# Kernel tuning notes

Hardware: AMD Instinct MI355X
Metric: run time of the kernel (lower is better)

The kernel has to match this reference:

```python
import jax, jax.numpy as jnp
import numpy as np
import math

B, S, D, H = 4, 2048, 1024, 16
HD = D // H  # 64


def setup_inputs() -> dict:
    key = jax.random.key(0)
    ks = jax.random.split(key, 12)
    s_in = 1.0 / math.sqrt(D)
    inp = {
        "x_v": jax.random.normal(ks[0], (B, S, D), jnp.float32),
        "x_k": jax.random.normal(ks[1], (B, S, D), jnp.float32),
        "x_q": jax.random.normal(ks[2], (B, S, D), jnp.float32),
        "mask": jax.random.randint(ks[3], (B, S, S), 0, 2, jnp.int32),
        "Wq": jax.random.normal(ks[4], (H, D, HD), jnp.float32) * s_in,
        "bq": jax.random.normal(ks[5], (H, HD), jnp.float32) * s_in,
        "Wk": jax.random.normal(ks[6], (H, D, HD), jnp.float32) * s_in,
        "bk": jax.random.normal(ks[7], (H, HD), jnp.float32) * s_in,
        "Wv": jax.random.normal(ks[8], (H, D, HD), jnp.float32) * s_in,
        "bv": jax.random.normal(ks[9], (H, HD), jnp.float32) * s_in,
        "Wo": jax.random.normal(ks[10], (D, D), jnp.float32) * s_in,
        "bo": jax.random.normal(ks[11], (D,), jnp.float32) * s_in,
    }
    return inp


def reference(x_v, x_k, x_q, mask, Wq, bq, Wk, bk, Wv, bv, Wo, bo):
    # Batched per-head projections: [B,S,D] x [H,D,E] -> [B,H,S,E]
    q = jnp.einsum("bsd,hde->bhse", x_q, Wq) + bq[None, :, None, :]
    k = jnp.einsum("bsd,hde->bhse", x_k, Wk) + bk[None, :, None, :]
    v = jnp.einsum("bsd,hde->bhse", x_v, Wv) + bv[None, :, None, :]
    scale = 1.0 / math.sqrt(HD)
    scores = jnp.einsum("bhqe,bhke->bhqk", q, k) * scale  # [B,H,Sq,Sk]
    # Faithful to original: masked positions are set to 0 (not -inf) BEFORE softmax
    scores = jnp.where(mask[:, None, :, :] == 0, 0.0, scores)
    attn = jax.nn.softmax(scores, axis=-1)
    z = jnp.einsum("bhqk,bhke->bhqe", attn, v)  # [B,H,Sq,E]
    # Concat over heads in head order (matches torch.cat along dim=2)
    z = z.transpose(0, 2, 1, 3).reshape(B, S, D)
    return z @ Wo + bo
```

## Files before the change

### kernel.cpp

```cpp
#include <hip/hip_runtime.h>

typedef unsigned short u16;
typedef unsigned long long u64;
typedef __attribute__((ext_vector_type(8))) short bf16x8;
typedef __attribute__((ext_vector_type(4))) float f32x4;

#define LD 72
#define C_SCALE 0.18033688011112043f

__device__ __forceinline__ u16 f2b(float x) {
  union { float f; unsigned u; } c; c.f = x;
  unsigned r = (c.u + 0x7fffu + ((c.u >> 16) & 1u)) >> 16;
  return (u16)r;
}

__device__ __forceinline__ unsigned pk2(float a, float b) {
#if __has_builtin(__builtin_amdgcn_cvt_pk_bf16_f32)
  typedef __attribute__((ext_vector_type(2))) __bf16 b2;
  b2 r = __builtin_amdgcn_cvt_pk_bf16_f32(a, b);
  union { b2 v; unsigned u; } c; c.v = r;
  return c.u;
#else
  union { float f; unsigned u; } x, y;
  x.f = a; y.f = b;
  return ((x.u + 0x8000u) >> 16) | ((y.u + 0x8000u) & 0xffff0000u);
#endif
}

__device__ __forceinline__ void gll16(const u16* g, u16* l) {
  __builtin_amdgcn_global_load_lds(
      (const __attribute__((address_space(1))) void*)g,
      (__attribute__((address_space(3))) void*)l, 16, 0, 0);
}

__global__ __launch_bounds__(256) void cvt_bf16_3(
    const float4* __restrict__ s0, const float4* __restrict__ s1,
    const float4* __restrict__ s2, ushort4* __restrict__ d0,
    ushort4* __restrict__ d1, ushort4* __restrict__ d2, int n4) {
  const int z = blockIdx.y;
  const float4* src = z == 0 ? s0 : z == 1 ? s1 : s2;
  ushort4* dst = z == 0 ? d0 : z == 1 ? d1 : d2;
  int stride = gridDim.x * 256;
  for (int i = blockIdx.x * 256 + threadIdx.x; i < n4; i += stride) {
    float4 v = src[i];
    ushort4 o = { f2b(v.x), f2b(v.y), f2b(v.z), f2b(v.w) };
    dst[i] = o;
  }
}

__global__ __launch_bounds__(256) void transpose_cvt_all(
    const float* __restrict__ Wq, const float* __restrict__ Wk,
    const float* __restrict__ Wv, const float* __restrict__ Wo,
    u16* __restrict__ wq_t, u16* __restrict__ wk_t,
    u16* __restrict__ wv_t, u16* __restrict__ wo_t) {
  __shared__ u16 tile[64][65];
  const int id = blockIdx.x;
  const int which = id >> 8, sub = id & 255;
  const float* s;
  u16* d;
  int R, C, r0, c0;
  if (which < 3) {
    const float* W = which == 0 ? Wq : which == 1 ? Wk : Wv;
    u16* D = which == 0 ? wq_t : which == 1 ? wk_t : wv_t;
    int h = sub >> 4, rt = sub & 15;
    s = W + (size_t)h * 1024 * 64;
    d = D + (size_t)h * 64 * 1024;
    R = 1024; C = 64; r0 = rt * 64; c0 = 0;
  } else {
    s = Wo; d = wo_t;
    R = 1024; C = 1024; r0 = ((sub >> 4) & 15) * 64; c0 = (sub & 15) * 64;
  }
  const int t = threadIdx.x;
#pragma unroll
  for (int rep = 0; rep < 16; ++rep) {
    int idx = rep * 256 + t;
    int i = idx >> 6, j = idx & 63;
    tile[j][i] = f2b(s[(size_t)(r0 + i) * C + c0 + j]);
  }
  __syncthreads();
#pragma unroll
  for (int rep = 0; rep < 16; ++rep) {
    int idx = rep * 256 + t;
    int jj = idx >> 6, ii = idx & 63;
    d[(size_t)(c0 + jj) * R + r0 + ii] = tile[jj][ii];
  }
}

__global__ __launch_bounds__(256) void pack_mask(
    const int* __restrict__ m, u64* __restrict__ mp) {
  const int nw = (gridDim.x * 256) >> 6;
  const int wid = (blockIdx.x * 256 + threadIdx.x) >> 6;
  const int lane = threadIdx.x & 63;
  const int total = 4 * 2048 * 32;
  for (int i = wid; i < total; i += nw) {
    int v = m[(size_t)i * 64 + lane];
    u64 bits = __ballot(v != 0);
    if (lane == 0) mp[i] = bits;
  }
}

__device__ __forceinline__ void gemm_core(
    const u16* __restrict__ A, const u16* __restrict__ W,
    u16* Asm, u16* Bsm, int s0, int n0, int wv, int lane,
    int m16, int q4, f32x4 acc[4][4]) {
  const int rsub = lane >> 3, csub = lane & 7;
  const int wr = (wv & 1) * 64, wc = (wv >> 1) * 64;
  for (int k0 = 0; k0 < 1024; k0 += 64) {
    __syncthreads();
#pragma unroll
    for (int i = 0; i < 4; ++i) {
      int chunk = wv * 4 + i;
      gll16(A + (size_t)(s0 + chunk * 8 + rsub) * 1024 + k0 + csub * 8,
            Asm + chunk * 512 + lane * 8);
      gll16(W + (size_t)(n0 + chunk * 8 + rsub) * 1024 + k0 + csub * 8,
            Bsm + chunk * 512 + lane * 8);
    }
    __syncthreads();
#pragma unroll
    for (int ks = 0; ks < 2; ++ks) {
      bf16x8 af[4], bfr[4];
#pragma unroll
      for (int i = 0; i < 4; ++i)
        af[i] = *(const bf16x8*)(Asm + (wr + i * 16 + m16) * 64 + ks * 32 + q4 * 8);
#pragma unroll
      for (int j = 0; j < 4; ++j)
        bfr[j] = *(const bf16x8*)(Bsm + (wc + j * 16 + m16) * 64 + ks * 32 + q4 * 8);
#pragma unroll
      for (int i = 0; i < 4; ++i)
#pragma unroll
        for (int j = 0; j < 4; ++j)
          acc[i][j] = __builtin_amdgcn_mfma_f32_16x16x32_bf16(af[i], bfr[j], acc[i][j], 0, 0, 0);
    }
  }
}

__global__ __launch_bounds__(256, 2) void qkv_gemm(
    const u16* __restrict__ xq, const u16* __restrict__ xk,
    const u16* __restrict__ xv, const u16* __restrict__ wq,
    const u16* __restrict__ wk, const u16* __restrict__ wv_,
    const float* __restrict__ bq, const float* __restrict__ bk,
    const float* __restrict__ bv, u16* __restrict__ qb,
    u16* __restrict__ kb, u16* __restrict__ vtb) {
  __shared__ u16 S[17408];
  u16* Asm = S;
  u16* Bsm = S + 8192;
  const int z = blockIdx.z;
  const u16* A = z == 0 ? xq : z == 1 ? xk : xv;
  const u16* W = z == 0 ? wq : z == 1 ? wk : wv_;
  const float* bias = z == 0 ? bq : z == 1 ? bk : bv;
  const int s0 = blockIdx.x * 128, n0 = blockIdx.y * 128;
  const int t = threadIdx.x, wvi = t >> 6, lane = t & 63;
  const int m16 = lane & 15, q4 = lane >> 4;
  const int wr = (wvi & 1) * 64, wc = (wvi >> 1) * 64;
  f32x4 acc[4][4];
#pragma unroll
  for (int i = 0; i < 4; ++i)
#pragma unroll
    for (int j = 0; j < 4; ++j) acc[i][j] = (f32x4){0.f, 0.f, 0.f, 0.f};

  gemm_core(A, W, Asm, Bsm, s0, n0, wvi, lane, m16, q4, acc);

  if (z < 2) {
    u16* out = z == 0 ? qb : kb;
    const float scale = z == 0 ? C_SCALE : 1.0f;
#pragma unroll
    for (int j = 0; j < 4; ++j) {
      int n = n0 + wc + j * 16 + m16;
      int h = n >> 6, e = n & 63;
      float bval = bias[n];
#pragma unroll
      for (int i = 0; i < 4; ++i)
#pragma unroll
        for (int r = 0; r < 4; ++r) {
          int s = s0 + wr + i * 16 + q4 * 4 + r;
          int bi = s >> 11, sl = s & 2047;
          out[((size_t)(bi * 16 + h) * 2048 + sl) * 64 + e] =
              f2b((acc[i][j][r] + bval) * scale);
        }
    }
  } else {
    __syncthreads();
#pragma unroll
    for (int j = 0; j < 4; ++j) {
      int nl = wc + j * 16 + m16;
      float bval = bias[n0 + nl];
#pragma unroll
      for (int i = 0; i < 4; ++i)
#pragma unroll
        for (int r = 0; r < 4; ++r)
          S[nl * 136 + wr + i * 16 + q4 * 4 + r] = f2b(acc[i][j][r] + bval);
    }
    __syncthreads();
    const int bi = s0 >> 11, sl0 = s0 & 2047;
#pragma unroll
    for (int rep = 0; rep < 8; ++rep) {
      int u = rep * 256 + t;
      int rr = u >> 4, cc = (u & 15) * 8;
      int n = n0 + rr, h = n >> 6, e = n & 63;
      *(int4*)(vtb + ((size_t)(bi * 16 + h) * 64 + e) * 2048 + sl0 + cc) =
          *(const int4*)(S + rr * 136 + cc);
    }
  }
}

__global__ __launch_bounds__(256, 2) void out_gemm(
    const u16* __restrict__ Z, const u16* __restrict__ Wot,
    const float* __restrict__ bo, float* __restrict__ out) {
  __shared__ u16 S[17408];
  u16* Asm = S;
  u16* Bsm = S + 8192;
  const int s0 = blockIdx.x * 128, n0 = blockIdx.y * 128;
  const int t = threadIdx.x, wvi = t >> 6, lane = t & 63;
  const int m16 = lane & 15, q4 = lane >> 4;
  const int wr = (wvi & 1) * 64, wc = (wvi >> 1) * 64;
  f32x4 acc[4][4];
#pragma unroll
  for (int i = 0; i < 4; ++i)
#pragma unroll
    for (int j = 0; j < 4; ++j) acc[i][j] = (f32x4){0.f, 0.f, 0.f, 0.f};

  gemm_core(Z, Wot, Asm, Bsm, s0, n0, wvi, lane, m16, q4, acc);

#pragma unroll
  for (int j = 0; j < 4; ++j) {
    int n = n0 + wc + j * 16 + m16;
    float bval = bo[n];
#pragma unroll
    for (int i = 0; i < 4; ++i)
#pragma unroll
      for (int r = 0; r < 4; ++r) {
        int s = s0 + wr + i * 16 + q4 * 4 + r;
        out[(size_t)s * 1024 + n] = acc[i][j][r] + bval;
      }
  }
}

__global__ __launch_bounds__(256, 4) void attn(
    const u16* __restrict__ qb, const u16* __restrict__ kb,
    const u16* __restrict__ vt, const u64* __restrict__ mp,
    u16* __restrict__ zb) {
  __shared__ u16 Kl[2][64 * LD];
  __shared__ u16 Vl[2][64 * LD];
  const int id = blockIdx.x;
  const int qi = id >> 6;
  const int bh = id & 63;
  const int b = bh >> 4, h = bh & 15;
  const int t = threadIdx.x, w = t >> 6, lane = t & 63;
  const int m16 = lane & 15, q4 = lane >> 4;
  const size_t bho = (size_t)bh * 2048;
  const u16* qp = qb + bho * 64;
  const u16* kp = kb + bho * 64;
  const u16* vp = vt + bho * 64;
  const int qbase = qi * 128 + w * 32;

  bf16x8 qa[2][2];
#pragma unroll
  for (int qg = 0; qg < 2; ++qg)
#pragma unroll
    for (int ks = 0; ks < 2; ++ks)
      qa[qg][ks] = *(const bf16x8*)(qp + (size_t)(qbase + qg * 16 + m16) * 64 + ks * 32 + q4 * 8);

  f32x4 oacc[2][4], lacc[2];
#pragma unroll
  for (int qg = 0; qg < 2; ++qg) {
    lacc[qg] = (f32x4){0.f, 0.f, 0.f, 0.f};
#pragma unroll
    for (int g = 0; g < 4; ++g) oacc[qg][g] = (f32x4){0.f, 0.f, 0.f, 0.f};
  }
  bf16x8 ones;
#pragma unroll
  for (int j = 0; j < 8; ++j) ones[j] = (short)0x3f80;

  const u64* mpq0 = mp + ((size_t)b * 2048 + qbase + m16) * 32;
  const u64* mpq1 = mp + ((size_t)b * 2048 + qbase + 16 + m16) * 32;

  const int ch = t & 7, rw = t >> 3;
  const int sK = (((rw >> 2) & 1) * 16) + (((rw >> 3) & 3) * 4) + (rw & 3);

  int4 pk0 = *(const int4*)(kp + (size_t)rw * 64 + ch * 8);
  int4 pk1 = *(const int4*)(kp + (size_t)(rw + 32) * 64 + ch * 8);
  int4 pv0 = *(const int4*)(vp + (size_t)rw * 2048 + ch * 8);
  int4 pv1 = *(const int4*)(vp + (size_t)(rw + 32) * 2048 + ch * 8);
  u64 mb0 = mpq0[0], mb1 = mpq1[0];
  *(int4*)(&Kl[0][sK * LD + ch * 8]) = pk0;
  *(int4*)(&Kl[0][(sK + 32) * LD + ch * 8]) = pk1;
  *(int4*)(&Vl[0][rw * LD + ch * 8]) = pv0;
  *(int4*)(&Vl[0][(rw + 32) * LD + ch * 8]) = pv1;
  __syncthreads();

  for (int kt = 0; kt < 32; ++kt) {
    const int cur = kt & 1;
    u64 nmb0, nmb1;
    if (kt < 31) {
      const int k0n = (kt + 1) * 64;
      pk0 = *(const int4*)(kp + (size_t)(k0n + rw) * 64 + ch * 8);
      pk1 = *(const int4*)(kp + (size_t)(k0n + rw + 32) * 64 + ch * 8);
      pv0 = *(const int4*)(vp + (size_t)rw * 2048 + k0n + ch * 8);
      pv1 = *(const int4*)(vp + (size_t)(rw + 32) * 2048 + k0n + ch * 8);
      nmb0 = mpq0[kt + 1];
      nmb1 = mpq1[kt + 1];
    }

#pragma unroll
    for (int bb = 0; bb < 2; ++bb) {
      bf16x8 kf00 = *(const bf16x8*)(&Kl[cur][(bb * 32 + m16) * LD + q4 * 8]);
      bf16x8 kf01 = *(const bf16x8*)(&Kl[cur][(bb * 32 + m16) * LD + 32 + q4 * 8]);
      bf16x8 kf10 = *(const bf16x8*)(&Kl[cur][(bb * 32 + 16 + m16) * LD + q4 * 8]);
      bf16x8 kf11 = *(const bf16x8*)(&Kl[cur][(bb * 32 + 16 + m16) * LD + 32 + q4 * 8]);
      const unsigned by0 = (unsigned)(mb0 >> (bb * 32 + q4 * 8)) & 0xFFu;
      const unsigned by1 = (unsigned)(mb1 >> (bb * 32 + q4 * 8)) & 0xFFu;
      bf16x8 pa[2];
#pragma unroll
      for (int qg = 0; qg < 2; ++qg) {
        f32x4 sa = (f32x4){0.f, 0.f, 0.f, 0.f};
        f32x4 sb = (f32x4){0.f, 0.f, 0.f, 0.f};
        sa = __builtin_amdgcn_mfma_f32_16x16x32_bf16(kf00, qa[qg][0], sa, 0, 0, 0);
        sa = __builtin_amdgcn_mfma_f32_16x16x32_bf16(kf01, qa[qg][1], sa, 0, 0, 0);
        sb = __builtin_amdgcn_mfma_f32_16x16x32_bf16(kf10, qa[qg][0], sb, 0, 0, 0);
        sb = __builtin_amdgcn_mfma_f32_16x16x32_bf16(kf11, qa[qg][1], sb, 0, 0, 0);
        const unsigned by = qg ? by1 : by0;
        float p[8];
#pragma unroll
        for (int r = 0; r < 4; ++r) {
          p[r] = __builtin_amdgcn_exp2f((by & (1u << r)) ? sa[r] : 0.f);
          p[4 + r] = __builtin_amdgcn_exp2f((by & (1u << (4 + r))) ? sb[r] : 0.f);
        }
        union { unsigned u[4]; bf16x8 v; } pu;
        pu.u[0] = pk2(p[0], p[1]);
        pu.u[1] = pk2(p[2], p[3]);
        pu.u[2] = pk2(p[4], p[5]);
        pu.u[3] = pk2(p[6], p[7]);
        pa[qg] = pu.v;
        lacc[qg] = __builtin_amdgcn_mfma_f32_16x16x32_bf16(pa[qg], ones, lacc[qg], 0, 0, 0);
      }
#pragma unroll
      for (int e = 0; e < 4; ++e) {
        bf16x8 vf = *(const bf16x8*)(&Vl[cur][(e * 16 + m16) * LD + bb * 32 + q4 * 8]);
        oacc[0][e] = __builtin_amdgcn_mfma_f32_16x16x32_bf16(pa[0], vf, oacc[0][e], 0, 0, 0);
        oacc[1][e] = __builtin_amdgcn_mfma_f32_16x16x32_bf16(pa[1], vf, oacc[1][e], 0, 0, 0);
      }
    }

    if (kt < 31) {
      const int nxt = cur ^ 1;
      *(int4*)(&Kl[nxt][sK * LD + ch * 8]) = pk0;
      *(int4*)(&Kl[nxt][(sK + 32) * LD + ch * 8]) = pk1;
      *(int4*)(&Vl[nxt][rw * LD + ch * 8]) = pv0;
      *(int4*)(&Vl[nxt][(rw + 32) * LD + ch * 8]) = pv1;
      mb0 = nmb0;
      mb1 = nmb1;
      __syncthreads();
    }
  }

#pragma unroll
  for (int qg = 0; qg < 2; ++qg) {
#pragma unroll
    for (int r = 0; r < 4; ++r) {
      float inv = 1.f / lacc[qg][r];
      size_t zr = ((size_t)b * 2048 + qbase + qg * 16 + q4 * 4 + r) * 1024 + h * 64;
#pragma unroll
      for (int e = 0; e < 4; ++e) {
        zb[zr + e * 16 + m16] = f2b(oacc[qg][e][r] * inv);
      }
    }
  }
}

extern "C" void kernel_launch(void* const* d_in, const int* in_sizes, int n_in,
                              void* d_out, int out_size, void* d_ws, size_t ws_size,
                              hipStream_t stream) {
  const float* x_v = (const float*)d_in[0];
  const float* x_k = (const float*)d_in[1];
  const float* x_q = (const float*)d_in[2];
  const int* mask = (const int*)d_in[3];
  const float* Wq = (const float*)d_in[4];
  const float* bq = (const float*)d_in[5];
  const float* Wk = (const float*)d_in[6];
  const float* bk = (const float*)d_in[7];
  const float* Wv = (const float*)d_in[8];
  const float* bv = (const float*)d_in[9];
  const float* Wo = (const float*)d_in[10];
  const float* bo = (const float*)d_in[11];
  float* out = (float*)d_out;

  char* ws = (char*)d_ws;
  size_t off = 0;
  auto alloc_u16 = [&](size_t n) {
    u16* p = (u16*)(ws + off);
    off += n * sizeof(u16);
    return p;
  };
  u16* wq_t = alloc_u16((size_t)16 * 64 * 1024);
  u16* wk_t = alloc_u16((size_t)16 * 64 * 1024);
  u16* wv_t = alloc_u16((size_t)16 * 64 * 1024);
  u16* wo_t = alloc_u16((size_t)1024 * 1024);
  u16* qb = alloc_u16((size_t)8192 * 1024);
  u16* kb = alloc_u16((size_t)8192 * 1024);
  u16* vtb = alloc_u16((size_t)8192 * 1024);
  u16* xq16 = alloc_u16((size_t)8192 * 1024);
  u16* xk16 = alloc_u16((size_t)8192 * 1024);
  u16* xv16 = alloc_u16((size_t)8192 * 1024);
  u64* mp = (u64*)(ws + off);
  off += (size_t)262144 * 8;
  u16* zb = xq16;

  transpose_cvt_all<<<dim3(1024), 256, 0, stream>>>(
      Wq, Wk, Wv, Wo, wq_t, wk_t, wv_t, wo_t);
  pack_mask<<<dim3(1024), 256, 0, stream>>>(mask, mp);
  const int n4 = 8192 * 1024 / 4;
  cvt_bf16_3<<<dim3(512, 3), 256, 0, stream>>>(
      (const float4*)x_q, (const float4*)x_k, (const float4*)x_v,
      (ushort4*)xq16, (ushort4*)xk16, (ushort4*)xv16, n4);
  qkv_gemm<<<dim3(64, 8, 3), 256, 0, stream>>>(
      xq16, xk16, xv16, wq_t, wk_t, wv_t, bq, bk, bv, qb, kb, vtb);
  attn<<<dim3(1024), 256, 0, stream>>>(qb, kb, vtb, mp, zb);
  out_gemm<<<dim3(64, 8), 256, 0, stream>>>(zb, wo_t, bo, out);
}
```

Before: 420.7 us.

## Expand mask to bf16 multipliers instead of packed bits in attention

Replaces the bit-packed mask with a bf16 mask expanded to 1.0 or 0.0 per element. The attention kernel now loads int4 mask vectors per tile and applies the mask by multiplying scores before exp2, instead of selecting on extracted bits. This removes the per-element shift-and-test work, but grows the mask from about 2 MB to about 32 MB, and every head re-reads it. The expanded mask reuses the freed xk16/xv16 workspace. The qkv_gemm occupancy hint is also raised from 2 to 3 blocks.

```diff
diff --git a/kernel.cpp b/kernel.cpp
--- a/kernel.cpp
+++ b/kernel.cpp
@@ -25,6 +25,13 @@
   x.f = a; y.f = b;
   return ((x.u + 0x8000u) >> 16) | ((y.u + 0x8000u) & 0xffff0000u);
 #endif
+}
+
+__device__ __forceinline__ float blo(int w) {
+  union { int i; float f; } c; c.i = w << 16; return c.f;
+}
+__device__ __forceinline__ float bhi(int w) {
+  union { int i; float f; } c; c.i = w & 0xffff0000; return c.f;
 }
 
 __device__ __forceinline__ void gll16(const u16* g, u16* l) {
@@ -86,16 +93,14 @@
   }
 }
 
-__global__ __launch_bounds__(256) void pack_mask(
-    const int* __restrict__ m, u64* __restrict__ mp) {
-  const int nw = (gridDim.x * 256) >> 6;
-  const int wid = (blockIdx.x * 256 + threadIdx.x) >> 6;
-  const int lane = threadIdx.x & 63;
-  const int total = 4 * 2048 * 32;
-  for (int i = wid; i < total; i += nw) {
-    int v = m[(size_t)i * 64 + lane];
-    u64 bits = __ballot(v != 0);
-    if (lane == 0) mp[i] = bits;
+__global__ __launch_bounds__(256) void expand_mask(
+    const int4* __restrict__ m, ushort4* __restrict__ mb, int n4) {
+  int stride = gridDim.x * 256;
+  for (int i = blockIdx.x * 256 + threadIdx.x; i < n4; i += stride) {
+    int4 v = m[i];
+    ushort4 o = { (u16)(v.x ? 0x3f80 : 0), (u16)(v.y ? 0x3f80 : 0),
+                  (u16)(v.z ? 0x3f80 : 0), (u16)(v.w ? 0x3f80 : 0) };
+    mb[i] = o;
   }
 }
 
@@ -134,7 +139,7 @@
   }
 }
 
-__global__ __launch_bounds__(256, 2) void qkv_gemm(
+__global__ __launch_bounds__(256, 3) void qkv_gemm(
     const u16* __restrict__ xq, const u16* __restrict__ xk,
     const u16* __restrict__ xv, const u16* __restrict__ wq,
     const u16* __restrict__ wk, const u16* __restrict__ wv_,
@@ -237,7 +242,7 @@
 
 __global__ __launch_bounds__(256, 4) void attn(
     const u16* __restrict__ qb, const u16* __restrict__ kb,
-    const u16* __restrict__ vt, const u64* __restrict__ mp,
+    const u16* __restrict__ vt, const u16* __restrict__ mk,
     u16* __restrict__ zb) {
   __shared__ u16 Kl[2][64 * LD];
   __shared__ u16 Vl[2][64 * LD];
@@ -271,8 +276,9 @@
 #pragma unroll
   for (int j = 0; j < 8; ++j) ones[j] = (short)0x3f80;
 
-  const u64* mpq0 = mp + ((size_t)b * 2048 + qbase + m16) * 32;
-  const u64* mpq1 = mp + ((size_t)b * 2048 + qbase + 16 + m16) * 32;
+  const u16* mrow[2];
+  mrow[0] = mk + ((size_t)b * 2048 + qbase + m16) * 2048;
+  mrow[1] = mk + ((size_t)b * 2048 + qbase + 16 + m16) * 2048;
 
   const int ch = t & 7, rw = t >> 3;
   const int sK = (((rw >> 2) & 1) * 16) + (((rw >> 3) & 3) * 4) + (rw & 3);
@@ -281,7 +287,12 @@
   int4 pk1 = *(const int4*)(kp + (size_t)(rw + 32) * 64 + ch * 8);
   int4 pv0 = *(const int4*)(vp + (size_t)rw * 2048 + ch * 8);
   int4 pv1 = *(const int4*)(vp + (size_t)(rw + 32) * 2048 + ch * 8);
-  u64 mb0 = mpq0[0], mb1 = mpq1[0];
+  int4 cm[2][2], nm[2][2];
+#pragma unroll
+  for (int qg = 0; qg < 2; ++qg)
+#pragma unroll
+    for (int bb = 0; bb < 2; ++bb)
+      cm[qg][bb] = *(const int4*)(mrow[qg] + bb * 32 + q4 * 8);
   *(int4*)(&Kl[0][sK * LD + ch * 8]) = pk0;
   *(int4*)(&Kl[0][(sK + 32) * LD + ch * 8]) = pk1;
   *(int4*)(&Vl[0][rw * LD + ch * 8]) = pv0;
@@ -290,15 +301,17 @@
 
   for (int kt = 0; kt < 32; ++kt) {
     const int cur = kt & 1;
-    u64 nmb0, nmb1;
     if (kt < 31) {
       const int k0n = (kt + 1) * 64;
       pk0 = *(const int4*)(kp + (size_t)(k0n + rw) * 64 + ch * 8);
       pk1 = *(const int4*)(kp + (size_t)(k0n + rw + 32) * 64 + ch * 8);
       pv0 = *(const int4*)(vp + (size_t)rw * 2048 + k0n + ch * 8);
       pv1 = *(const int4*)(vp + (size_t)(rw + 32) * 2048 + k0n + ch * 8);
-      nmb0 = mpq0[kt + 1];
-      nmb1 = mpq1[kt + 1];
+#pragma unroll
+      for (int qg = 0; qg < 2; ++qg)
+#pragma unroll
+        for (int bb = 0; bb < 2; ++bb)
+          nm[qg][bb] = *(const int4*)(mrow[qg] + k0n + bb * 32 + q4 * 8);
     }
 
 #pragma unroll
@@ -307,8 +320,6 @@
       bf16x8 kf01 = *(const bf16x8*)(&Kl[cur][(bb * 32 + m16) * LD + 32 + q4 * 8]);
       bf16x8 kf10 = *(const bf16x8*)(&Kl[cur][(bb * 32 + 16 + m16) * LD + q4 * 8]);
       bf16x8 kf11 = *(const bf16x8*)(&Kl[cur][(bb * 32 + 16 + m16) * LD + 32 + q4 * 8]);
-      const unsigned by0 = (unsigned)(mb0 >> (bb * 32 + q4 * 8)) & 0xFFu;
-      const unsigned by1 = (unsigned)(mb1 >> (bb * 32 + q4 * 8)) & 0xFFu;
       bf16x8 pa[2];
 #pragma unroll
       for (int qg = 0; qg < 2; ++qg) {
@@ -318,13 +329,16 @@
         sa = __builtin_amdgcn_mfma_f32_16x16x32_bf16(kf01, qa[qg][1], sa, 0, 0, 0);
         sb = __builtin_amdgcn_mfma_f32_16x16x32_bf16(kf10, qa[qg][0], sb, 0, 0, 0);
         sb = __builtin_amdgcn_mfma_f32_16x16x32_bf16(kf11, qa[qg][1], sb, 0, 0, 0);
-        const unsigned by = qg ? by1 : by0;
+        const int4 mw = cm[qg][bb];
         float p[8];
-#pragma unroll
-        for (int r = 0; r < 4; ++r) {
-          p[r] = __builtin_amdgcn_exp2f((by & (1u << r)) ? sa[r] : 0.f);
-          p[4 + r] = __builtin_amdgcn_exp2f((by & (1u << (4 + r))) ? sb[r] : 0.f);
-        }
+        p[0] = __builtin_amdgcn_exp2f(sa[0] * blo(mw.x));
+        p[1] = __builtin_amdgcn_exp2f(sa[1] * bhi(mw.x));
+        p[2] = __builtin_amdgcn_exp2f(sa[2] * blo(mw.y));
+        p[3] = __builtin_amdgcn_exp2f(sa[3] * bhi(mw.y));
+        p[4] = __builtin_amdgcn_exp2f(sb[0] * blo(mw.z));
+        p[5] = __builtin_amdgcn_exp2f(sb[1] * bhi(mw.z));
+        p[6] = __builtin_amdgcn_exp2f(sb[2] * blo(mw.w));
+        p[7] = __builtin_amdgcn_exp2f(sb[3] * bhi(mw.w));
         union { unsigned u[4]; bf16x8 v; } pu;
         pu.u[0] = pk2(p[0], p[1]);
         pu.u[1] = pk2(p[2], p[3]);
@@ -347,8 +361,10 @@
       *(int4*)(&Kl[nxt][(sK + 32) * LD + ch * 8]) = pk1;
       *(int4*)(&Vl[nxt][rw * LD + ch * 8]) = pv0;
       *(int4*)(&Vl[nxt][(rw + 32) * LD + ch * 8]) = pv1;
-      mb0 = nmb0;
-      mb1 = nmb1;
+#pragma unroll
+      for (int qg = 0; qg < 2; ++qg)
+#pragma unroll
+        for (int bb = 0; bb < 2; ++bb) cm[qg][bb] = nm[qg][bb];
       __syncthreads();
     }
   }
@@ -401,19 +417,19 @@
   u16* xq16 = alloc_u16((size_t)8192 * 1024);
   u16* xk16 = alloc_u16((size_t)8192 * 1024);
   u16* xv16 = alloc_u16((size_t)8192 * 1024);
-  u64* mp = (u64*)(ws + off);
-  off += (size_t)262144 * 8;
   u16* zb = xq16;
+  u16* mask16 = xk16;
 
   transpose_cvt_all<<<dim3(1024), 256, 0, stream>>>(
       Wq, Wk, Wv, Wo, wq_t, wk_t, wv_t, wo_t);
-  pack_mask<<<dim3(1024), 256, 0, stream>>>(mask, mp);
   const int n4 = 8192 * 1024 / 4;
   cvt_bf16_3<<<dim3(512, 3), 256, 0, stream>>>(
       (const float4*)x_q, (const float4*)x_k, (const float4*)x_v,
       (ushort4*)xq16, (ushort4*)xk16, (ushort4*)xv16, n4);
   qkv_gemm<<<dim3(64, 8, 3), 256, 0, stream>>>(
       xq16, xk16, xv16, wq_t, wk_t, wv_t, bq, bk, bv, qb, kb, vtb);
-  attn<<<dim3(1024), 256, 0, stream>>>(qb, kb, vtb, mp, zb);
+  expand_mask<<<dim3(2048), 256, 0, stream>>>(
+      (const int4*)mask, (ushort4*)mask16, 4 * 2048 * 2048 / 4);
+  attn<<<dim3(1024), 256, 0, stream>>>(qb, kb, vtb, mask16, zb);
   out_gemm<<<dim3(64, 8), 256, 0, stream>>>(zb, wo_t, bo, out);
 }
```

New measurement: 402.4 us. -4.3%, faster.
